# Optimization experiments

Measured on AMD Instinct MI355X. Metric: run time of the kernel, lower is better.

Reference implementation:

```python
import jax, jax.numpy as jnp
import numpy as np

E = 768
H = 12
D = E // H
K = 512  # max_relative_positions
SCALE = 1.0 / np.sqrt(3.0 * D)


def setup_inputs() -> dict:
    key = jax.random.key(0)
    ks = jax.random.split(key, 14)
    B, S = 4, 1024
    def lin(kw):
        return jax.random.normal(kw, (E, E), dtype=jnp.float32) * 0.02
    inp = {
        "x": jax.random.normal(ks[0], (B, S, E), dtype=jnp.float32),
        "Wq": lin(ks[1]), "bq": jnp.zeros((E,), jnp.float32),
        "Wk": lin(ks[2]), "bk": jnp.zeros((E,), jnp.float32),
        "Wv": lin(ks[3]), "bv": jnp.zeros((E,), jnp.float32),
        "Wpq": lin(ks[4]), "bpq": jnp.zeros((E,), jnp.float32),
        "Wpk": lin(ks[5]), "bpk": jnp.zeros((E,), jnp.float32),
        "rel_emb": jax.random.normal(ks[6], (2 * K + 1, E), dtype=jnp.float32) * 0.02,
        "Wo": lin(ks[7]), "bo": jnp.zeros((E,), jnp.float32),
    }
    return inp


def reference(x, Wq, bq, Wk, bk, Wv, bv, Wpq, bpq, Wpk, bpk, rel_emb, Wo, bo):
    B, S, _ = x.shape

    def split_heads(y):  # [B,S,E] -> [B,H,S,D]
        return y.reshape(B, S, H, D).transpose(0, 2, 1, 3)

    q_c = split_heads(x @ Wq.T + bq)
    k_c = split_heads(x @ Wk.T + bk)
    v = split_heads(x @ Wv.T + bv)

    # positional projections: [2K+1, E] -> [H, 2K+1, D]
    q_r = (rel_emb @ Wpq.T + bpq).reshape(2 * K + 1, H, D).transpose(1, 0, 2)
    k_r = (rel_emb @ Wpk.T + bpk).reshape(2 * K + 1, H, D).transpose(1, 0, 2)

    # relative index: rel[i, j] = clip(j - i, -K, K) + K
    pos = jnp.arange(S)
    rel = jnp.clip(pos[None, :] - pos[:, None], -K, K) + K  # [S, S] int32
    rel_b = jnp.broadcast_to(rel[None, None], (B, H, S, S))

    # content-to-content: [B,H,S,S]
    attn_cc = jnp.einsum('bhid,bhjd->bhij', q_c, k_c)

    # content-to-position: scores over all 2K+1 rel positions, then gather
    cp_score = jnp.einsum('bhid,hjd->bhij', q_c, k_r)  # [B,H,S,2K+1]
    attn_cp = jnp.take_along_axis(cp_score, rel_b, axis=-1)  # [B,H,S,S]

    # position-to-content: gather along last dim then transpose (i<->j)
    pc_score = jnp.einsum('bhjd,hkd->bhjk', k_c, q_r)  # [B,H,S,2K+1]
    attn_pc = jnp.take_along_axis(pc_score, rel_b, axis=-1).swapaxes(-1, -2)

    scores = (attn_cc + attn_cp + attn_pc) * SCALE
    weights = jax.nn.softmax(scores, axis=-1)

    ctx = jnp.einsum('bhij,bhjd->bhid', weights, v)
    ctx = ctx.transpose(0, 2, 1, 3).reshape(B, S, E)
    return ctx @ Wo.T + bo
```

## Files before the change

### kernel.cpp

```cpp
#include <hip/hip_runtime.h>
#include <stdint.h>

typedef __attribute__((ext_vector_type(8))) short bf8_t;
typedef __attribute__((ext_vector_type(4))) float f4_t;

#define DEV __device__ __forceinline__

constexpr int S_ = 1024;
constexpr float SCALE2_ = 0.104117584f;

DEV float bf2f(unsigned short u) { union { unsigned int i; float f; } v; v.i = ((unsigned int)u) << 16; return v.f; }
DEV unsigned short f2bf(float f) {
  union { float fv; unsigned int i; } v; v.fv = f;
  unsigned int r = v.i + 0x7FFFu + ((v.i >> 16) & 1u);
  return (unsigned short)(r >> 16);
}

DEV void gll16(const unsigned short* g, unsigned short* l) {
  __builtin_amdgcn_global_load_lds(
      (const __attribute__((address_space(1))) unsigned int*)g,
      (__attribute__((address_space(3))) unsigned int*)l, 16, 0, 0);
}

DEV const bf8_t* chunk128(const unsigned short* base, int row, int ck) {
  return (const bf8_t*)((const char*)base + row * 128 + (((ck ^ row) & 7) << 4));
}

struct CvtArgs { const float* src[8]; unsigned short* dst[8]; int nchunks[8]; };

__global__ __launch_bounds__(256) void cvt_kernel(CvtArgs a, int total) {
  int idx = blockIdx.x * 256 + threadIdx.x;
  int step = gridDim.x * 256;
  for (; idx < total; idx += step) {
    int c = idx, s = 0;
    while (c >= a.nchunks[s]) { c -= a.nchunks[s]; ++s; }
    float4 v = ((const float4*)a.src[s])[c];
    ushort4 o;
    o.x = f2bf(v.x); o.y = f2bf(v.y); o.z = f2bf(v.z); o.w = f2bf(v.w);
    ((ushort4*)a.dst[s])[c] = o;
  }
}

enum { MQKVF = 0, MRELF = 1, MOUT = 2 };

template <int MODE>
__global__ __launch_bounds__(256) void gemm_bt(
    const unsigned short* __restrict__ A, int lda,
    const unsigned short* __restrict__ B, int ldb,
    void* __restrict__ C,
    const float* __restrict__ b0, const float* __restrict__ b1, const float* __restrict__ b2,
    int M, int N, int Kd)
{
  __shared__ unsigned short At[64 * 64];
  __shared__ unsigned short Bt[128 * 64];
  const int tid = threadIdx.x, lane = tid & 63, w = tid >> 6;
  const int li = lane & 15, g = lane >> 4;
  const int wr = w >> 1, wc = w & 1;
  const int m0 = blockIdx.y * 64, n0 = blockIdx.x * 128;

  const int srow = tid >> 3;
  const int sl = (tid & 7) ^ (srow & 7);
  const long aoff0 = (long)min(m0 + srow,      M - 1) * lda + sl * 8;
  const long aoff1 = (long)min(m0 + srow + 32, M - 1) * lda + sl * 8;
  const long boff0 = (long)min(n0 + srow,      N - 1) * ldb + sl * 8;
  const long boff1 = (long)min(n0 + srow + 32, N - 1) * ldb + sl * 8;
  const long boff2 = (long)min(n0 + srow + 64, N - 1) * ldb + sl * 8;
  const long boff3 = (long)min(n0 + srow + 96, N - 1) * ldb + sl * 8;

  f4_t acc[2][4];
#pragma unroll
  for (int i = 0; i < 2; ++i)
#pragma unroll
    for (int j = 0; j < 4; ++j) acc[i][j] = f4_t{0.f, 0.f, 0.f, 0.f};

  for (int k0 = 0; k0 < Kd; k0 += 64) {
    gll16(A + aoff0 + k0, At + tid * 8);
    gll16(A + aoff1 + k0, At + tid * 8 + 2048);
    gll16(B + boff0 + k0, Bt + tid * 8);
    gll16(B + boff1 + k0, Bt + tid * 8 + 2048);
    gll16(B + boff2 + k0, Bt + tid * 8 + 4096);
    gll16(B + boff3 + k0, Bt + tid * 8 + 6144);
    asm volatile("s_waitcnt vmcnt(0)" ::: "memory");
    __syncthreads();

#pragma unroll
    for (int ks = 0; ks < 2; ++ks) {
      bf8_t a[2], b[4];
#pragma unroll
      for (int fm = 0; fm < 2; ++fm)
        a[fm] = *chunk128(At, wr * 32 + fm * 16 + li, ks * 4 + g);
#pragma unroll
      for (int fn = 0; fn < 4; ++fn)
        b[fn] = *chunk128(Bt, wc * 64 + fn * 16 + li, ks * 4 + g);
#pragma unroll
      for (int fm = 0; fm < 2; ++fm)
#pragma unroll
        for (int fn = 0; fn < 4; ++fn)
          acc[fm][fn] = __builtin_amdgcn_mfma_f32_16x16x32_bf16(a[fm], b[fn], acc[fm][fn], 0, 0, 0);
    }
    __syncthreads();
  }

#pragma unroll
  for (int fm = 0; fm < 2; ++fm)
#pragma unroll
    for (int fn = 0; fn < 4; ++fn)
#pragma unroll
      for (int r = 0; r < 4; ++r) {
        int row = wr * 32 + fm * 16 + g * 4 + r;
        int col = wc * 64 + fn * 16 + li;
        int m = m0 + row, n = n0 + col;
        if (m >= M || n >= N) continue;
        float v = acc[fm][fn][r];
        if constexpr (MODE == MQKVF) {
          int sel = (n >= 1536) ? 2 : (n >= 768 ? 1 : 0);
          int nn = n - sel * 768;
          v += (sel == 0 ? b0 : sel == 1 ? b1 : b2)[nn];
          long off = (long)sel * 3145728 + (long)((m >> 10) * 12 + (nn >> 6)) * 65536;
          if (sel == 2) off += (nn & 63) * 1024 + (m & 1023);
          else          off += (m & 1023) * 64 + (nn & 63);
          ((unsigned short*)C)[off] = f2bf(v);
        } else if constexpr (MODE == MRELF) {
          int sel = n >= 768 ? 1 : 0;
          int nn = n - sel * 768;
          v += (sel ? b1 : b0)[nn];
          long off = (long)sel * 787200 + (long)(nn >> 6) * 65600 + (long)m * 64 + (nn & 63);
          ((unsigned short*)C)[off] = f2bf(v);
        } else {
          v += b0[n];
          ((float*)C)[(long)m * 768 + n] = v;
        }
      }
}

__global__ __launch_bounds__(256) void flash_kernel(
    const unsigned short* __restrict__ Q, const unsigned short* __restrict__ Kc,
    const unsigned short* __restrict__ kr, const unsigned short* __restrict__ qr,
    const unsigned short* __restrict__ Vt, unsigned short* __restrict__ ctx)
{
  const int flat = blockIdx.x;
  const int logical = (flat & 7) * 96 + (flat >> 3);
  const int bh = logical >> 4, h = bh % 12, bb = bh / 12;
  const int i0 = (logical & 15) * 64;
  const int tid = threadIdx.x, lane = tid & 63, w = tid >> 6;
  const int g = lane >> 4, li = lane & 15;
  const unsigned short* Qb  = Q  + (long)bh * (S_ * 64);
  const unsigned short* Kb  = Kc + (long)bh * (S_ * 64);
  const unsigned short* Vb  = Vt + (long)bh * (S_ * 64);
  const unsigned short* krh = kr + (long)h * 65600;
  const unsigned short* qrh = qr + (long)h * 65600;

  __shared__ unsigned short Kt[4096];
  __shared__ unsigned short Vl[4096];
  __shared__ unsigned short Tpc[64][132];
  __shared__ unsigned short TcpW[4][16][84];
  __shared__ unsigned short Pl[4096];

  const int mh = w & 1, nq = w >> 1;

  const int sr0 = w * 8 + (lane >> 3);
  const int scc = (lane & 7) ^ (sr0 & 7);
  auto stage = [&](int jt) {
    const int j0n = jt * 64;
    gll16(Kb + (long)(j0n + sr0) * 64 + scc * 8,        &Kt[w * 512 + lane * 8]);
    gll16(Kb + (long)(j0n + sr0 + 32) * 64 + scc * 8,   &Kt[w * 512 + 2048 + lane * 8]);
    gll16(Vb + (long)sr0 * 1024 + j0n + scc * 8,        &Vl[w * 512 + lane * 8]);
    gll16(Vb + (long)(sr0 + 32) * 1024 + j0n + scc * 8, &Vl[w * 512 + 2048 + lane * 8]);
  };

  bf8_t q3[2];
#pragma unroll
  for (int ks = 0; ks < 2; ++ks)
    q3[ks] = *(const bf8_t*)(Qb + (long)(i0 + w * 16 + li) * 64 + ks * 32 + g * 8);

  float l_p[4] = {0.f, 0.f, 0.f, 0.f};
  f4_t acc_o[4];
#pragma unroll
  for (int fn = 0; fn < 4; ++fn) acc_o[fn] = f4_t{0.f, 0.f, 0.f, 0.f};

  const int base_cp = li + 15 - g * 4;
  const int base_pc = 63 + w * 16 + g * 4 - li;

  stage(0);

  for (int jt = 0; jt < 16; ++jt) {
    const int j0 = jt * 64;
    const int Dl = j0 - i0;
    const int wbU = Dl - w * 16 - 15 + 512;
    const int rbU = 449 - Dl;

    {
      f4_t at[5];
#pragma unroll
      for (int f5 = 0; f5 < 5; ++f5) at[f5] = f4_t{0.f, 0.f, 0.f, 0.f};
#pragma unroll
      for (int ks = 0; ks < 2; ++ks) {
        bf8_t b[5];
#pragma unroll
        for (int f5 = 0; f5 < 5; ++f5) {
          int krow = min(max(wbU + f5 * 16 + li, 0), 1024);
          b[f5] = *(const bf8_t*)(krh + (long)krow * 64 + ks * 32 + g * 8);
        }
#pragma unroll
        for (int f5 = 0; f5 < 5; ++f5)
          at[f5] = __builtin_amdgcn_mfma_f32_16x16x32_bf16(q3[ks], b[f5], at[f5], 0, 0, 0);
      }
#pragma unroll
      for (int f5 = 0; f5 < 5; ++f5)
#pragma unroll
        for (int r = 0; r < 4; ++r)
          TcpW[w][g * 4 + r][f5 * 16 + li] = f2bf(at[f5][r]);
    }

    asm volatile("s_waitcnt vmcnt(0)" ::: "memory");
    __builtin_amdgcn_s_barrier();

    {
      f4_t acc[2][4];
#pragma unroll
      for (int i = 0; i < 2; ++i)
#pragma unroll
        for (int j = 0; j < 4; ++j) acc[i][j] = f4_t{0.f, 0.f, 0.f, 0.f};
#pragma unroll
      for (int ks = 0; ks < 2; ++ks) {
        bf8_t a[2], b[4];
#pragma unroll
        for (int fm = 0; fm < 2; ++fm)
          a[fm] = *chunk128(Kt, mh * 32 + fm * 16 + li, ks * 4 + g);
#pragma unroll
        for (int fn = 0; fn < 4; ++fn) {
          int qrow = min(max(rbU + nq * 64 + fn * 16 + li, 0), 1024);
          b[fn] = *(const bf8_t*)(qrh + (long)qrow * 64 + ks * 32 + g * 8);
        }
#pragma unroll
        for (int fm = 0; fm < 2; ++fm)
#pragma unroll
          for (int fn = 0; fn < 4; ++fn)
            acc[fm][fn] = __builtin_amdgcn_mfma_f32_16x16x32_bf16(a[fm], b[fn], acc[fm][fn], 0, 0, 0);
      }
#pragma unroll
      for (int fm = 0; fm < 2; ++fm)
#pragma unroll
        for (int fn = 0; fn < 4; ++fn)
#pragma unroll
          for (int r = 0; r < 4; ++r)
            Tpc[mh * 32 + fm * 16 + g * 4 + r][nq * 64 + fn * 16 + li] = f2bf(acc[fm][fn][r]);
    }

    asm volatile("s_waitcnt lgkmcnt(0)" ::: "memory");
    __builtin_amdgcn_s_barrier();

    f4_t s4[4];
#pragma unroll
    for (int fn = 0; fn < 4; ++fn) s4[fn] = f4_t{0.f, 0.f, 0.f, 0.f};
#pragma unroll
    for (int ks = 0; ks < 2; ++ks) {
      bf8_t b[4];
#pragma unroll
      for (int fn = 0; fn < 4; ++fn)
        b[fn] = *chunk128(Kt, fn * 16 + li, ks * 4 + g);
#pragma unroll
      for (int fn = 0; fn < 4; ++fn)
        s4[fn] = __builtin_amdgcn_mfma_f32_16x16x32_bf16(q3[ks], b[fn], s4[fn], 0, 0, 0);
    }

#pragma unroll
    for (int fn = 0; fn < 4; ++fn)
#pragma unroll
      for (int r = 0; r < 4; ++r) {
        float v = s4[fn][r] + bf2f(TcpW[w][g * 4 + r][base_cp + fn * 16 - r])
                            + bf2f(Tpc[fn * 16 + li][base_pc + r - fn * 16]);
        float p = exp2f(v * SCALE2_);
        l_p[r] += p;
        const int row = w * 16 + g * 4 + r;
        int byte = row * 128 + (fn * 16 + li) * 2;
        byte ^= (row & 7) << 4;
        *(unsigned short*)((char*)Pl + byte) = f2bf(p);
      }

#pragma unroll
    for (int ks = 0; ks < 2; ++ks) {
      const int arow = w * 16 + li;
      int abyte = arow * 128 + ks * 64 + g * 16;
      abyte ^= (arow & 7) << 4;
      bf8_t a = *(const bf8_t*)((const char*)Pl + abyte);
      bf8_t b[4];
#pragma unroll
      for (int fn2 = 0; fn2 < 4; ++fn2)
        b[fn2] = *chunk128(Vl, fn2 * 16 + li, ks * 4 + g);
#pragma unroll
      for (int fn2 = 0; fn2 < 4; ++fn2)
        acc_o[fn2] = __builtin_amdgcn_mfma_f32_16x16x32_bf16(a, b[fn2], acc_o[fn2], 0, 0, 0);
    }

    if (jt + 1 < 16) {
      __builtin_amdgcn_s_barrier();
      stage(jt + 1);
    }
  }

#pragma unroll
  for (int r = 0; r < 4; ++r)
#pragma unroll
    for (int off = 1; off < 16; off <<= 1) l_p[r] += __shfl_xor(l_p[r], off);
  float inv[4];
#pragma unroll
  for (int r = 0; r < 4; ++r) inv[r] = 1.0f / l_p[r];
#pragma unroll
  for (int fn2 = 0; fn2 < 4; ++fn2)
#pragma unroll
    for (int r = 0; r < 4; ++r) {
      const int row = i0 + w * 16 + g * 4 + r;
      const int d = fn2 * 16 + li;
      float v = acc_o[fn2][r] * inv[r];
      ctx[((long)bb * 1024 + row) * 768 + h * 64 + d] = f2bf(v);
    }
}

extern "C" void kernel_launch(void* const* d_in, const int* in_sizes, int n_in,
                              void* d_out, int out_size, void* d_ws, size_t ws_size,
                              hipStream_t stream)
{
  const float* x   = (const float*)d_in[0];
  const float* Wq  = (const float*)d_in[1];
  const float* bq  = (const float*)d_in[2];
  const float* Wk  = (const float*)d_in[3];
  const float* bk  = (const float*)d_in[4];
  const float* Wv  = (const float*)d_in[5];
  const float* bv  = (const float*)d_in[6];
  const float* Wpq = (const float*)d_in[7];
  const float* bpq = (const float*)d_in[8];
  const float* Wpk = (const float*)d_in[9];
  const float* bpk = (const float*)d_in[10];
  const float* rel = (const float*)d_in[11];
  const float* Wo  = (const float*)d_in[12];
  const float* bo  = (const float*)d_in[13];

  char* ws = (char*)d_ws;
  auto alloc = [&](size_t bytes) { char* p = ws; ws += (bytes + 255) & ~(size_t)255; return p; };
  unsigned short* xb   = (unsigned short*)alloc((size_t)4096 * 768 * 2);
  unsigned short* Wqb  = (unsigned short*)alloc((size_t)768 * 768 * 2);
  unsigned short* Wkb  = (unsigned short*)alloc((size_t)768 * 768 * 2);
  unsigned short* Wvb  = (unsigned short*)alloc((size_t)768 * 768 * 2);
  unsigned short* Wpqb = (unsigned short*)alloc((size_t)768 * 768 * 2);
  unsigned short* Wpkb = (unsigned short*)alloc((size_t)768 * 768 * 2);
  unsigned short* Wob  = (unsigned short*)alloc((size_t)768 * 768 * 2);
  unsigned short* relb = (unsigned short*)alloc((size_t)1025 * 768 * 2);
  unsigned short* Qb   = (unsigned short*)alloc((size_t)48 * 1024 * 64 * 2);
  unsigned short* Kb   = (unsigned short*)alloc((size_t)48 * 1024 * 64 * 2);
  unsigned short* Vt   = (unsigned short*)alloc((size_t)48 * 64 * 1024 * 2);
  unsigned short* qkx  = (unsigned short*)alloc((size_t)2 * 12 * 1025 * 64 * 2);
  unsigned short* ctx  = (unsigned short*)alloc((size_t)4096 * 768 * 2);

  CvtArgs ca;
  const float* srcs[8] = {x, Wq, Wk, Wv, Wpq, Wpk, Wo, rel};
  unsigned short* dsts[8] = {xb, Wqb, Wkb, Wvb, Wpqb, Wpkb, Wob, relb};
  const int nch[8] = {786432, 147456, 147456, 147456, 147456, 147456, 147456, 196800};
  int total = 0;
  for (int i = 0; i < 8; ++i) { ca.src[i] = srcs[i]; ca.dst[i] = dsts[i]; ca.nchunks[i] = nch[i]; total += nch[i]; }
  cvt_kernel<<<dim3(2048), dim3(256), 0, stream>>>(ca, total);

  dim3 blk(256);
  gemm_bt<MQKVF><<<dim3(18, 64), blk, 0, stream>>>(xb, 768, Wqb, 768, Qb, bq, bk, bv, 4096, 2304, 768);
  gemm_bt<MRELF><<<dim3(12, 17), blk, 0, stream>>>(relb, 768, Wpqb, 768, qkx, bpq, bpk, nullptr, 1025, 1536, 768);
  flash_kernel<<<dim3(768), blk, 0, stream>>>(Qb, Kb, qkx + 787200, qkx, Vt, ctx);
  gemm_bt<MOUT><<<dim3(6, 64), blk, 0, stream>>>(ctx, 768, Wob, 768, d_out, bo, nullptr, nullptr, 4096, 768, 768);

  (void)in_sizes; (void)n_in; (void)out_size; (void)ws_size;
}
```

Before: 205.9 us.

## Merge QKV and relative-position GEMMs into one launch; add MFMA priority hints

Merges the QKV projection GEMM and the relative-embedding projection GEMM into one grid launch so the small rel GEMM fills SMs alongside the large one, and removes one kernel launch. The output GEMM becomes its own specialized kernel without bounds clamps. In the flash kernel, the position-to-content GEMM now reads K directly from global memory rather than from shared memory, which drops one barrier and its wait. s_setprio is also placed around the MFMA bursts to favour the matrix issue. The direct global reads of K may add latency or cache traffic.

```diff
diff --git a/kernel.cpp b/kernel.cpp
--- a/kernel.cpp
+++ b/kernel.cpp
@@ -41,31 +41,35 @@
   }
 }
 
-enum { MQKVF = 0, MRELF = 1, MOUT = 2 };
-
-template <int MODE>
-__global__ __launch_bounds__(256) void gemm_bt(
-    const unsigned short* __restrict__ A, int lda,
-    const unsigned short* __restrict__ B, int ldb,
-    void* __restrict__ C,
-    const float* __restrict__ b0, const float* __restrict__ b1, const float* __restrict__ b2,
-    int M, int N, int Kd)
+__global__ __launch_bounds__(256) void gemm_qkvrel(
+    const unsigned short* __restrict__ xb, const unsigned short* __restrict__ Wqkv,
+    const unsigned short* __restrict__ relb, const unsigned short* __restrict__ Wrel,
+    unsigned short* __restrict__ Cqkv, unsigned short* __restrict__ Crel,
+    const float* __restrict__ bq, const float* __restrict__ bk, const float* __restrict__ bv,
+    const float* __restrict__ bpq, const float* __restrict__ bpk)
 {
   __shared__ unsigned short At[64 * 64];
   __shared__ unsigned short Bt[128 * 64];
   const int tid = threadIdx.x, lane = tid & 63, w = tid >> 6;
   const int li = lane & 15, g = lane >> 4;
   const int wr = w >> 1, wc = w & 1;
-  const int m0 = blockIdx.y * 64, n0 = blockIdx.x * 128;
+
+  const int bid = blockIdx.x;
+  const bool qkv = bid < 1152;
+  const unsigned short *A, *B;
+  int m0, n0, M, N;
+  if (qkv) { m0 = (bid / 18) * 64; n0 = (bid % 18) * 128; A = xb;   B = Wqkv; M = 4096; N = 2304; }
+  else     { int t = bid - 1152;
+             m0 = (t / 12) * 64;  n0 = (t % 12) * 128;  A = relb; B = Wrel; M = 1025; N = 1536; }
 
   const int srow = tid >> 3;
   const int sl = (tid & 7) ^ (srow & 7);
-  const long aoff0 = (long)min(m0 + srow,      M - 1) * lda + sl * 8;
-  const long aoff1 = (long)min(m0 + srow + 32, M - 1) * lda + sl * 8;
-  const long boff0 = (long)min(n0 + srow,      N - 1) * ldb + sl * 8;
-  const long boff1 = (long)min(n0 + srow + 32, N - 1) * ldb + sl * 8;
-  const long boff2 = (long)min(n0 + srow + 64, N - 1) * ldb + sl * 8;
-  const long boff3 = (long)min(n0 + srow + 96, N - 1) * ldb + sl * 8;
+  const long aoff0 = (long)min(m0 + srow,      M - 1) * 768 + sl * 8;
+  const long aoff1 = (long)min(m0 + srow + 32, M - 1) * 768 + sl * 8;
+  const long boff0 = (long)min(n0 + srow,      N - 1) * 768 + sl * 8;
+  const long boff1 = (long)min(n0 + srow + 32, N - 1) * 768 + sl * 8;
+  const long boff2 = (long)min(n0 + srow + 64, N - 1) * 768 + sl * 8;
+  const long boff3 = (long)min(n0 + srow + 96, N - 1) * 768 + sl * 8;
 
   f4_t acc[2][4];
 #pragma unroll
@@ -73,7 +77,7 @@
 #pragma unroll
     for (int j = 0; j < 4; ++j) acc[i][j] = f4_t{0.f, 0.f, 0.f, 0.f};
 
-  for (int k0 = 0; k0 < Kd; k0 += 64) {
+  for (int k0 = 0; k0 < 768; k0 += 64) {
     gll16(A + aoff0 + k0, At + tid * 8);
     gll16(A + aoff1 + k0, At + tid * 8 + 2048);
     gll16(B + boff0 + k0, Bt + tid * 8);
@@ -82,7 +86,6 @@
     gll16(B + boff3 + k0, Bt + tid * 8 + 6144);
     asm volatile("s_waitcnt vmcnt(0)" ::: "memory");
     __syncthreads();
-
 #pragma unroll
     for (int ks = 0; ks < 2; ++ks) {
       bf8_t a[2], b[4];
@@ -107,29 +110,91 @@
     for (int fn = 0; fn < 4; ++fn)
 #pragma unroll
       for (int r = 0; r < 4; ++r) {
-        int row = wr * 32 + fm * 16 + g * 4 + r;
-        int col = wc * 64 + fn * 16 + li;
-        int m = m0 + row, n = n0 + col;
+        int m = m0 + wr * 32 + fm * 16 + g * 4 + r;
+        int n = n0 + wc * 64 + fn * 16 + li;
         if (m >= M || n >= N) continue;
         float v = acc[fm][fn][r];
-        if constexpr (MODE == MQKVF) {
+        if (qkv) {
           int sel = (n >= 1536) ? 2 : (n >= 768 ? 1 : 0);
           int nn = n - sel * 768;
-          v += (sel == 0 ? b0 : sel == 1 ? b1 : b2)[nn];
+          v += (sel == 0 ? bq : sel == 1 ? bk : bv)[nn];
           long off = (long)sel * 3145728 + (long)((m >> 10) * 12 + (nn >> 6)) * 65536;
           if (sel == 2) off += (nn & 63) * 1024 + (m & 1023);
           else          off += (m & 1023) * 64 + (nn & 63);
-          ((unsigned short*)C)[off] = f2bf(v);
-        } else if constexpr (MODE == MRELF) {
+          Cqkv[off] = f2bf(v);
+        } else {
           int sel = n >= 768 ? 1 : 0;
           int nn = n - sel * 768;
-          v += (sel ? b1 : b0)[nn];
+          v += (sel ? bpk : bpq)[nn];
           long off = (long)sel * 787200 + (long)(nn >> 6) * 65600 + (long)m * 64 + (nn & 63);
-          ((unsigned short*)C)[off] = f2bf(v);
-        } else {
-          v += b0[n];
-          ((float*)C)[(long)m * 768 + n] = v;
+          Crel[off] = f2bf(v);
         }
+      }
+}
+
+__global__ __launch_bounds__(256) void gemm_out(
+    const unsigned short* __restrict__ A,
+    const unsigned short* __restrict__ B,
+    float* __restrict__ C, const float* __restrict__ b0)
+{
+  __shared__ unsigned short At[64 * 64];
+  __shared__ unsigned short Bt[128 * 64];
+  const int tid = threadIdx.x, lane = tid & 63, w = tid >> 6;
+  const int li = lane & 15, g = lane >> 4;
+  const int wr = w >> 1, wc = w & 1;
+  const int m0 = blockIdx.y * 64, n0 = blockIdx.x * 128;
+
+  const int srow = tid >> 3;
+  const int sl = (tid & 7) ^ (srow & 7);
+  const long aoff0 = (long)(m0 + srow) * 768 + sl * 8;
+  const long aoff1 = (long)(m0 + srow + 32) * 768 + sl * 8;
+  const long boff0 = (long)(n0 + srow) * 768 + sl * 8;
+  const long boff1 = (long)(n0 + srow + 32) * 768 + sl * 8;
+  const long boff2 = (long)(n0 + srow + 64) * 768 + sl * 8;
+  const long boff3 = (long)(n0 + srow + 96) * 768 + sl * 8;
+
+  f4_t acc[2][4];
+#pragma unroll
+  for (int i = 0; i < 2; ++i)
+#pragma unroll
+    for (int j = 0; j < 4; ++j) acc[i][j] = f4_t{0.f, 0.f, 0.f, 0.f};
+
+  for (int k0 = 0; k0 < 768; k0 += 64) {
+    gll16(A + aoff0 + k0, At + tid * 8);
+    gll16(A + aoff1 + k0, At + tid * 8 + 2048);
+    gll16(B + boff0 + k0, Bt + tid * 8);
+    gll16(B + boff1 + k0, Bt + tid * 8 + 2048);
+    gll16(B + boff2 + k0, Bt + tid * 8 + 4096);
+    gll16(B + boff3 + k0, Bt + tid * 8 + 6144);
+    asm volatile("s_waitcnt vmcnt(0)" ::: "memory");
+    __syncthreads();
+#pragma unroll
+    for (int ks = 0; ks < 2; ++ks) {
+      bf8_t a[2], b[4];
+#pragma unroll
+      for (int fm = 0; fm < 2; ++fm)
+        a[fm] = *chunk128(At, wr * 32 + fm * 16 + li, ks * 4 + g);
+#pragma unroll
+      for (int fn = 0; fn < 4; ++fn)
+        b[fn] = *chunk128(Bt, wc * 64 + fn * 16 + li, ks * 4 + g);
+#pragma unroll
+      for (int fm = 0; fm < 2; ++fm)
+#pragma unroll
+        for (int fn = 0; fn < 4; ++fn)
+          acc[fm][fn] = __builtin_amdgcn_mfma_f32_16x16x32_bf16(a[fm], b[fn], acc[fm][fn], 0, 0, 0);
+    }
+    __syncthreads();
+  }
+
+#pragma unroll
+  for (int fm = 0; fm < 2; ++fm)
+#pragma unroll
+    for (int fn = 0; fn < 4; ++fn)
+#pragma unroll
+      for (int r = 0; r < 4; ++r) {
+        int m = m0 + wr * 32 + fm * 16 + g * 4 + r;
+        int n = n0 + wc * 64 + fn * 16 + li;
+        C[(long)m * 768 + n] = acc[fm][fn][r] + b0[n];
       }
 }
 
@@ -201,21 +266,18 @@
           int krow = min(max(wbU + f5 * 16 + li, 0), 1024);
           b[f5] = *(const bf8_t*)(krh + (long)krow * 64 + ks * 32 + g * 8);
         }
+        __builtin_amdgcn_s_setprio(1);
 #pragma unroll
         for (int f5 = 0; f5 < 5; ++f5)
           at[f5] = __builtin_amdgcn_mfma_f32_16x16x32_bf16(q3[ks], b[f5], at[f5], 0, 0, 0);
+        __builtin_amdgcn_s_setprio(0);
       }
 #pragma unroll
       for (int f5 = 0; f5 < 5; ++f5)
 #pragma unroll
         for (int r = 0; r < 4; ++r)
           TcpW[w][g * 4 + r][f5 * 16 + li] = f2bf(at[f5][r]);
-    }
-
-    asm volatile("s_waitcnt vmcnt(0)" ::: "memory");
-    __builtin_amdgcn_s_barrier();
-
-    {
+
       f4_t acc[2][4];
 #pragma unroll
       for (int i = 0; i < 2; ++i)
@@ -226,17 +288,19 @@
         bf8_t a[2], b[4];
 #pragma unroll
         for (int fm = 0; fm < 2; ++fm)
-          a[fm] = *chunk128(Kt, mh * 32 + fm * 16 + li, ks * 4 + g);
+          a[fm] = *(const bf8_t*)(Kb + (long)(j0 + mh * 32 + fm * 16 + li) * 64 + ks * 32 + g * 8);
 #pragma unroll
         for (int fn = 0; fn < 4; ++fn) {
           int qrow = min(max(rbU + nq * 64 + fn * 16 + li, 0), 1024);
           b[fn] = *(const bf8_t*)(qrh + (long)qrow * 64 + ks * 32 + g * 8);
         }
+        __builtin_amdgcn_s_setprio(1);
 #pragma unroll
         for (int fm = 0; fm < 2; ++fm)
 #pragma unroll
           for (int fn = 0; fn < 4; ++fn)
             acc[fm][fn] = __builtin_amdgcn_mfma_f32_16x16x32_bf16(a[fm], b[fn], acc[fm][fn], 0, 0, 0);
+        __builtin_amdgcn_s_setprio(0);
       }
 #pragma unroll
       for (int fm = 0; fm < 2; ++fm)
@@ -247,7 +311,7 @@
             Tpc[mh * 32 + fm * 16 + g * 4 + r][nq * 64 + fn * 16 + li] = f2bf(acc[fm][fn][r]);
     }
 
-    asm volatile("s_waitcnt lgkmcnt(0)" ::: "memory");
+    asm volatile("s_waitcnt vmcnt(0) lgkmcnt(0)" ::: "memory");
     __builtin_amdgcn_s_barrier();
 
     f4_t s4[4];
@@ -259,9 +323,11 @@
 #pragma unroll
       for (int fn = 0; fn < 4; ++fn)
         b[fn] = *chunk128(Kt, fn * 16 + li, ks * 4 + g);
+      __builtin_amdgcn_s_setprio(1);
 #pragma unroll
       for (int fn = 0; fn < 4; ++fn)
         s4[fn] = __builtin_amdgcn_mfma_f32_16x16x32_bf16(q3[ks], b[fn], s4[fn], 0, 0, 0);
+      __builtin_amdgcn_s_setprio(0);
     }
 
 #pragma unroll
@@ -288,9 +354,11 @@
 #pragma unroll
       for (int fn2 = 0; fn2 < 4; ++fn2)
         b[fn2] = *chunk128(Vl, fn2 * 16 + li, ks * 4 + g);
+      __builtin_amdgcn_s_setprio(1);
 #pragma unroll
       for (int fn2 = 0; fn2 < 4; ++fn2)
         acc_o[fn2] = __builtin_amdgcn_mfma_f32_16x16x32_bf16(a, b[fn2], acc_o[fn2], 0, 0, 0);
+      __builtin_amdgcn_s_setprio(0);
     }
 
     if (jt + 1 < 16) {
@@ -361,10 +429,10 @@
   cvt_kernel<<<dim3(2048), dim3(256), 0, stream>>>(ca, total);
 
   dim3 blk(256);
-  gemm_bt<MQKVF><<<dim3(18, 64), blk, 0, stream>>>(xb, 768, Wqb, 768, Qb, bq, bk, bv, 4096, 2304, 768);
-  gemm_bt<MRELF><<<dim3(12, 17), blk, 0, stream>>>(relb, 768, Wpqb, 768, qkx, bpq, bpk, nullptr, 1025, 1536, 768);
+  gemm_qkvrel<<<dim3(1356), blk, 0, stream>>>(xb, Wqb, relb, Wpqb, Qb, qkx,
+                                              bq, bk, bv, bpq, bpk);
   flash_kernel<<<dim3(768), blk, 0, stream>>>(Qb, Kb, qkx + 787200, qkx, Vt, ctx);
-  gemm_bt<MOUT><<<dim3(6, 64), blk, 0, stream>>>(ctx, 768, Wob, 768, d_out, bo, nullptr, nullptr, 4096, 768, 768);
+  gemm_out<<<dim3(6, 64), blk, 0, stream>>>(ctx, Wob, (float*)d_out, bo);
 
   (void)in_sizes; (void)n_in; (void)out_size; (void)ws_size;
 }
```

After: 202.3 us. About the same (-1.7%).
